# Performance work log

Hardware: AMD Instinct MI355X
Metric: run time of the kernel (lower is better)

Reference implementation:

```python
import jax, jax.numpy as jnp
import numpy as np

N, NF1, NF2, NH, OUT, K = 16384, 2000, 10000, 512, 16, 19
BN_EPS = 1e-5

def _bn(x, g, b, m, v):
    # eval-mode BatchNorm1d with running stats
    return (x - m) * jax.lax.rsqrt(v + BN_EPS) * g + b


def setup_inputs() -> dict:
    key = jax.random.key(0)
    ks = jax.random.split(key, 24)
    f32 = jnp.float32
    def w(k, shape):
        return jax.random.normal(k, shape, f32) * 0.02
    inp = {
        "rna": jax.random.normal(ks[0], (N, NF1), f32),
        "atac": jax.random.normal(ks[1], (N, NF2), f32),
        "index_rna": jnp.arange(N, dtype=jnp.int32),
        "index_atac": jnp.arange(N, dtype=jnp.int32),
        "eps": jax.random.normal(ks[2], (N, OUT), f32),
        # RNA encoder
        "W_r1": w(ks[3], (NH, NF1)), "b_r1": jnp.zeros((NH,), f32),
        "g_r": jnp.ones((NH,), f32), "be_r": jnp.zeros((NH,), f32),
        "m_r": jnp.zeros((NH,), f32), "v_r": jnp.ones((NH,), f32),
        "W_rmu": w(ks[4], (OUT, NH)), "b_rmu": jnp.zeros((OUT,), f32),
        "W_rvar": w(ks[5], (OUT, NH)), "b_rvar": jnp.zeros((OUT,), f32),
        # ATAC encoder
        "W_a1": w(ks[6], (NH, NF2)), "b_a1": jnp.zeros((NH,), f32),
        "g_a": jnp.ones((NH,), f32), "be_a": jnp.zeros((NH,), f32),
        "m_a": jnp.zeros((NH,), f32), "v_a": jnp.ones((NH,), f32),
        "W_amu": w(ks[7], (OUT, NH)), "b_amu": jnp.zeros((OUT,), f32),
        "W_avar": w(ks[8], (OUT, NH)), "b_avar": jnp.zeros((OUT,), f32),
        # decoder
        "W_d1": w(ks[9], (NH, OUT)), "b_d1": jnp.zeros((NH,), f32),
        "g_d": jnp.ones((NH,), f32), "be_d": jnp.zeros((NH,), f32),
        "m_d": jnp.zeros((NH,), f32), "v_d": jnp.ones((NH,), f32),
        "W_d4": w(ks[10], (NF1 + NF2, NH)), "b_d4": jnp.zeros((NF1 + NF2,), f32),
        "cluster": jax.random.normal(ks[11], (K, OUT), f32),
    }
    return inp


def reference(rna, atac, index_rna, index_atac, eps,
              W_r1, b_r1, g_r, be_r, m_r, v_r, W_rmu, b_rmu, W_rvar, b_rvar,
              W_a1, b_a1, g_a, be_a, m_a, v_a, W_amu, b_amu, W_avar, b_avar,
              W_d1, b_d1, g_d, be_d, m_d, v_d, W_d4, b_d4, cluster):
    n = rna.shape[0]
    # encoders (dropout is identity in eval mode)
    h_rna = jax.nn.relu(_bn(rna @ W_r1.T + b_r1, g_r, be_r, m_r, v_r))
    zm_rna = h_rna @ W_rmu.T + b_rmu
    zv_rna = jnp.exp(h_rna @ W_rvar.T + b_rvar)
    h_atac = jax.nn.relu(_bn(atac @ W_a1.T + b_a1, g_a, be_a, m_a, v_a))
    zm_atac = h_atac @ W_amu.T + b_amu
    zv_atac = jnp.exp(h_atac @ W_avar.T + b_avar)
    # vectorized scatter replacing the per-sample Python loop
    mu = jnp.ones((n, 2, OUT), rna.dtype)
    var = jnp.ones((n, 2, OUT), rna.dtype)
    mask = jnp.zeros((n, 2, OUT), rna.dtype)
    mu = mu.at[index_rna, 0].set(zm_rna).at[index_atac, 1].set(zm_atac)
    var = var.at[index_rna, 0].set(zv_rna).at[index_atac, 1].set(zv_atac)
    mask = mask.at[index_rna, 0].set(1.0).at[index_atac, 1].set(1.0)
    # product of experts over the modality axis (axis=1)
    T = mask / var
    T_sum = T.sum(axis=1) + 1.0            # [n, OUT]
    z_mu = (mu * T).sum(axis=1) / T_sum
    z_var = 1.0 / T_sum
    # Normal(z_mu, scale=z_var).rsample() with externally supplied eps
    z = z_mu + z_var * eps
    # student-t style soft assignment to clusters
    d2 = jnp.sum((z[:, None, :] - cluster[None, :, :]) ** 2, axis=2)  # [n, K]
    q = 1.0 / (1.0 + d2)
    q = q / q.sum(axis=1, keepdims=True)
    # decoder
    h = jax.nn.relu(_bn(z @ W_d1.T + b_d1, g_d, be_d, m_d, v_d))
    recon_x = h @ W_d4.T + b_d4
    return (recon_x, z_mu, z_var, z, q)
```

## Files before the change

kernel.cpp:

```cpp
#include <hip/hip_runtime.h>

#define NS   16384
#define NF1c 2000
#define NF2c 10000
#define NH   512
#define KC   19
#define NREC 12000

typedef short bf16x8 __attribute__((ext_vector_type(8)));
typedef float f32x4  __attribute__((ext_vector_type(4)));

__device__ __forceinline__ unsigned short f2bf(float x) {
    unsigned int u = __builtin_bit_cast(unsigned int, x);
    u += 0x7FFFu + ((u >> 16) & 1u);
    return (unsigned short)(u >> 16);
}
__device__ __forceinline__ float bf2f(unsigned short h) {
    return __builtin_bit_cast(float, (unsigned int)h << 16);
}

__global__ void k_cvt(const float* __restrict__ s, unsigned short* __restrict__ d, int n4) {
    int i = blockIdx.x * blockDim.x + threadIdx.x;
    int st = gridDim.x * blockDim.x;
    for (; i < n4; i += st) {
        float4 f = ((const float4*)s)[i];
        ushort4 o;
        o.x = f2bf(f.x); o.y = f2bf(f.y); o.z = f2bf(f.z); o.w = f2bf(f.w);
        ((ushort4*)d)[i] = o;
    }
}

__global__ void k_prep_st(const float* __restrict__ g, const float* __restrict__ be,
                          const float* __restrict__ m, const float* __restrict__ v,
                          const float* __restrict__ b1,
                          float* __restrict__ s, float* __restrict__ t, int n) {
    int i = blockIdx.x * blockDim.x + threadIdx.x;
    if (i < n) {
        float sc = g[i] * rsqrtf(v[i] + 1e-5f);
        s[i] = sc;
        t[i] = be[i] + (b1[i] - m[i]) * sc;
    }
}

__global__ void k_zero(float* __restrict__ p, int n) {
    int i = blockIdx.x * blockDim.x + threadIdx.x;
    if (i < n) p[i] = 0.f;
}

template<int EPI, int A_BF16>
__global__ __launch_bounds__(256)
void k_gemm(const void* __restrict__ Aptr, const unsigned short* __restrict__ B,
            int K, int Nn,
            const float* __restrict__ sc, const float* __restrict__ sh,
            unsigned short* __restrict__ Hout, float* __restrict__ Fout)
{
    __shared__ __align__(16) unsigned short As[128 * 32];
    __shared__ __align__(16) unsigned short Bs[128 * 32];
    const int tid  = threadIdx.x;
    const int tn   = blockIdx.x, tm = blockIdx.y;
    const int wave = tid >> 6, lane = tid & 63;
    const int wr   = wave >> 1, wc = wave & 1;
    const int lo   = lane & 15, hi = lane >> 4;
    const int srow = tid >> 1, shalf = tid & 1;
    const long arow = (long)tm * 128 + srow;
    const int  brow = tn * 128 + srow;

    f32x4 acc[4][4];
#pragma unroll
    for (int i = 0; i < 4; i++)
#pragma unroll
        for (int j = 0; j < 4; j++) acc[i][j] = (f32x4){0.f, 0.f, 0.f, 0.f};

    char* Ab = (char*)As;
    char* Bb = (char*)Bs;
    const int wc0 = (srow << 6) + ((((shalf * 2)    ) ^ ((srow >> 1) & 3)) << 4);
    const int wc1 = (srow << 6) + ((((shalf * 2) + 1) ^ ((srow >> 1) & 3)) << 4);

    for (int k0 = 0; k0 < K; k0 += 32) {
        __syncthreads();
        const int kb = k0 + shalf * 16;
        {
            __align__(16) unsigned short u[16];
            if (A_BF16) {
                const unsigned short* ap = (const unsigned short*)Aptr + arow * (long)K + kb;
                *(uint4*)&u[0] = *(const uint4*)(ap);
                *(uint4*)&u[8] = *(const uint4*)(ap + 8);
            } else {
                const float* ap = (const float*)Aptr + arow * (long)K + kb;
                if (kb + 16 <= K) {
#pragma unroll
                    for (int q = 0; q < 4; q++) {
                        float4 f = ((const float4*)ap)[q];
                        u[q*4+0] = f2bf(f.x); u[q*4+1] = f2bf(f.y);
                        u[q*4+2] = f2bf(f.z); u[q*4+3] = f2bf(f.w);
                    }
                } else {
#pragma unroll
                    for (int j = 0; j < 16; j++)
                        u[j] = (kb + j < K) ? f2bf(ap[j]) : (unsigned short)0;
                }
            }
            *(uint4*)(Ab + wc0) = *(uint4*)&u[0];
            *(uint4*)(Ab + wc1) = *(uint4*)&u[8];
        }
        {
            uint4 q0 = {0, 0, 0, 0}, q1 = {0, 0, 0, 0};
            if (brow < Nn && kb < K) {
                const unsigned short* bp = B + (long)brow * K + kb;
                if (kb + 16 <= K) {
                    q0 = *(const uint4*)bp;
                    q1 = *(const uint4*)(bp + 8);
                } else {
                    __align__(16) unsigned short tb[16];
#pragma unroll
                    for (int j = 0; j < 16; j++)
                        tb[j] = (kb + j < K) ? bp[j] : (unsigned short)0;
                    q0 = *(uint4*)&tb[0]; q1 = *(uint4*)&tb[8];
                }
            }
            *(uint4*)(Bb + wc0) = q0;
            *(uint4*)(Bb + wc1) = q1;
        }
        __syncthreads();
        bf16x8 af[4], bfr[4];
#pragma unroll
        for (int f = 0; f < 4; f++) {
            int ar = wr * 64 + f * 16 + lo;
            af[f]  = *(const bf16x8*)(Ab + (ar << 6) + ((hi ^ ((ar >> 1) & 3)) << 4));
            int br = wc * 64 + f * 16 + lo;
            bfr[f] = *(const bf16x8*)(Bb + (br << 6) + ((hi ^ ((br >> 1) & 3)) << 4));
        }
#pragma unroll
        for (int i = 0; i < 4; i++)
#pragma unroll
            for (int j = 0; j < 4; j++)
                acc[i][j] = __builtin_amdgcn_mfma_f32_16x16x32_bf16(af[i], bfr[j], acc[i][j], 0, 0, 0);
    }
#pragma unroll
    for (int i = 0; i < 4; i++) {
#pragma unroll
        for (int j = 0; j < 4; j++) {
            const int col = tn * 128 + wc * 64 + j * 16 + lo;
#pragma unroll
            for (int r = 0; r < 4; r++) {
                const long row = (long)tm * 128 + wr * 64 + i * 16 + hi * 4 + r;
                float v = acc[i][j][r];
                if (EPI == 0) {
                    v = fmaxf(v * sc[col] + sh[col], 0.f);
                    Hout[row * NH + col] = f2bf(v);
                } else {
                    if (col < Nn) Fout[row * (long)Nn + col] = v + sc[col];
                }
            }
        }
    }
}

__global__ __launch_bounds__(256)
void k_proj(const unsigned short* __restrict__ h_rna,
            const unsigned short* __restrict__ h_atac,
            const float* __restrict__ W_rmu, const float* __restrict__ b_rmu,
            const float* __restrict__ W_rvar, const float* __restrict__ b_rvar,
            const float* __restrict__ W_amu, const float* __restrict__ b_amu,
            const float* __restrict__ W_avar, const float* __restrict__ b_avar,
            const int* __restrict__ idx_rna, const int* __restrict__ idx_atac,
            float* __restrict__ mu0, float* __restrict__ var0,
            float* __restrict__ mu1, float* __restrict__ var1,
            float* __restrict__ mflag)
{
    __shared__ __align__(16) unsigned short hsh[4][2][NH];
    const int wave = threadIdx.x >> 6, lane = threadIdx.x & 63;
    const long i = (long)blockIdx.x * 4 + wave;
    *(uint4*)&hsh[wave][0][lane * 8] = *(const uint4*)(h_rna  + i * NH + lane * 8);
    *(uint4*)&hsh[wave][1][lane * 8] = *(const uint4*)(h_atac + i * NH + lane * 8);
    __syncthreads();
    const int mod = lane >> 5, oo = lane & 31;
    const int isv = oo >> 4, o = oo & 15;
    const float *W, *bias;
    if (mod == 0) { W = isv ? W_rvar : W_rmu; bias = isv ? b_rvar : b_rmu; }
    else          { W = isv ? W_avar : W_amu; bias = isv ? b_avar : b_amu; }
    const unsigned short* hr = hsh[wave][mod];
    const float* wrow = W + o * NH;
    float a = 0.f;
#pragma unroll 4
    for (int k = 0; k < NH; k += 4) {
        float4 w = *(const float4*)(wrow + k);
        a += bf2f(hr[k]) * w.x + bf2f(hr[k+1]) * w.y + bf2f(hr[k+2]) * w.z + bf2f(hr[k+3]) * w.w;
    }
    a += bias[o];
    const int tgt = (mod == 0) ? idx_rna[i] : idx_atac[i];
    float* mu  = mod ? mu1  : mu0;
    float* var = mod ? var1 : var0;
    if (!isv) mu[(long)tgt * 16 + o] = a;
    else      var[(long)tgt * 16 + o] = expf(a);
    if (oo == 0) mflag[(long)mod * NS + tgt] = 1.f;
}

__global__ __launch_bounds__(256)
void k_combine(const float* __restrict__ mu0, const float* __restrict__ var0,
               const float* __restrict__ mu1, const float* __restrict__ var1,
               const float* __restrict__ mflag,
               const float* __restrict__ eps, const float* __restrict__ cluster,
               const float* __restrict__ W_d1,
               const float* __restrict__ s_d, const float* __restrict__ t_d,
               float* __restrict__ o_zmu, float* __restrict__ o_zvar,
               float* __restrict__ o_z, float* __restrict__ o_q,
               unsigned short* __restrict__ h_d)
{
    __shared__ float zsh[4][16];
    const int wave = threadIdx.x >> 6, lane = threadIdx.x & 63;
    const long i = (long)blockIdx.x * 4 + wave;
    if (lane < 16) {
        const int d = lane;
        const float f0 = mflag[i], f1 = mflag[NS + i];
        float ts = 1.f, num = 0.f;
        if (f0 != 0.f) { float iv = 1.f / var0[i*16+d]; ts += iv; num += mu0[i*16+d] * iv; }
        if (f1 != 0.f) { float iv = 1.f / var1[i*16+d]; ts += iv; num += mu1[i*16+d] * iv; }
        const float zm = num / ts, zv = 1.f / ts;
        const float z = zm + zv * eps[i*16+d];
        o_zmu[i*16+d] = zm; o_zvar[i*16+d] = zv; o_z[i*16+d] = z;
        zsh[wave][d] = z;
    }
    __syncthreads();
    float zreg[16];
#pragma unroll
    for (int d = 0; d < 16; d++) zreg[d] = zsh[wave][d];
    float qk = 0.f;
    if (lane < KC) {
        float d2 = 0.f;
#pragma unroll
        for (int d = 0; d < 16; d++) { float df = zreg[d] - cluster[lane*16+d]; d2 += df*df; }
        qk = 1.f / (1.f + d2);
    }
    float ssum = qk;
#pragma unroll
    for (int off = 16; off > 0; off >>= 1) ssum += __shfl_xor(ssum, off, 32);
    if (lane < KC) o_q[i * KC + lane] = qk / ssum;
#pragma unroll
    for (int j = 0; j < 8; j++) {
        const int c = lane + 64 * j;
        float a = 0.f;
#pragma unroll
        for (int d = 0; d < 16; d += 4) {
            float4 w = *(const float4*)(W_d1 + c * 16 + d);
            a += zreg[d] * w.x + zreg[d+1] * w.y + zreg[d+2] * w.z + zreg[d+3] * w.w;
        }
        a = fmaxf(a * s_d[c] + t_d[c], 0.f);
        h_d[i * NH + c] = f2bf(a);
    }
}

extern "C" void kernel_launch(void* const* d_in, const int* in_sizes, int n_in,
                              void* d_out, int out_size, void* d_ws, size_t ws_size,
                              hipStream_t stream)
{
    const float* rna    = (const float*)d_in[0];
    const float* atac   = (const float*)d_in[1];
    const int*   i_rna  = (const int*)d_in[2];
    const int*   i_atac = (const int*)d_in[3];
    const float* eps    = (const float*)d_in[4];
    const float* W_r1   = (const float*)d_in[5];
    const float* b_r1   = (const float*)d_in[6];
    const float* g_r    = (const float*)d_in[7];
    const float* be_r   = (const float*)d_in[8];
    const float* m_r    = (const float*)d_in[9];
    const float* v_r    = (const float*)d_in[10];
    const float* W_rmu  = (const float*)d_in[11];
    const float* b_rmu  = (const float*)d_in[12];
    const float* W_rvar = (const float*)d_in[13];
    const float* b_rvar = (const float*)d_in[14];
    const float* W_a1   = (const float*)d_in[15];
    const float* b_a1   = (const float*)d_in[16];
    const float* g_a    = (const float*)d_in[17];
    const float* be_a   = (const float*)d_in[18];
    const float* m_a    = (const float*)d_in[19];
    const float* v_a    = (const float*)d_in[20];
    const float* W_amu  = (const float*)d_in[21];
    const float* b_amu  = (const float*)d_in[22];
    const float* W_avar = (const float*)d_in[23];
    const float* b_avar = (const float*)d_in[24];
    const float* W_d1   = (const float*)d_in[25];
    const float* b_d1   = (const float*)d_in[26];
    const float* g_d    = (const float*)d_in[27];
    const float* be_d   = (const float*)d_in[28];
    const float* m_d    = (const float*)d_in[29];
    const float* v_d    = (const float*)d_in[30];
    const float* W_d4   = (const float*)d_in[31];
    const float* b_d4   = (const float*)d_in[32];
    const float* clus   = (const float*)d_in[33];
    (void)in_sizes; (void)n_in; (void)out_size;

    char* w = (char*)d_ws;
    size_t off = 0;
    auto carve = [&](size_t bytes) { void* p = w + off; off += (bytes + 255) & ~(size_t)255; return p; };
    unsigned short* wr1b  = (unsigned short*)carve((size_t)NH * NF1c * 2);
    unsigned short* wa1b  = (unsigned short*)carve((size_t)NH * NF2c * 2);
    unsigned short* wd4b  = (unsigned short*)carve((size_t)NREC * NH * 2);
    unsigned short* hrna  = (unsigned short*)carve((size_t)NS * NH * 2);
    unsigned short* hatac = (unsigned short*)carve((size_t)NS * NH * 2);
    unsigned short* hd    = (unsigned short*)carve((size_t)NS * NH * 2);
    float* mu0   = (float*)carve((size_t)NS * 16 * 4);
    float* var0  = (float*)carve((size_t)NS * 16 * 4);
    float* mu1   = (float*)carve((size_t)NS * 16 * 4);
    float* var1  = (float*)carve((size_t)NS * 16 * 4);
    float* mflag = (float*)carve((size_t)2 * NS * 4);
    float* st    = (float*)carve((size_t)6 * NH * 4);
    if (off > ws_size) return;

    float* s_r = st;          float* t_r = st + NH;
    float* s_a = st + 2*NH;   float* t_a = st + 3*NH;
    float* s_d = st + 4*NH;   float* t_d = st + 5*NH;

    float* out    = (float*)d_out;
    float* o_rec  = out;
    float* o_zmu  = out + (size_t)NS * NREC;
    float* o_zvar = o_zmu + (size_t)NS * 16;
    float* o_z    = o_zvar + (size_t)NS * 16;
    float* o_q    = o_z + (size_t)NS * 16;

    k_cvt<<<1024, 256, 0, stream>>>(W_r1, wr1b, NH * NF1c / 4);
    k_cvt<<<2048, 256, 0, stream>>>(W_a1, wa1b, NH * NF2c / 4);
    k_cvt<<<2048, 256, 0, stream>>>(W_d4, wd4b, NREC * NH / 4);
    k_prep_st<<<2, 256, 0, stream>>>(g_r, be_r, m_r, v_r, b_r1, s_r, t_r, NH);
    k_prep_st<<<2, 256, 0, stream>>>(g_a, be_a, m_a, v_a, b_a1, s_a, t_a, NH);
    k_prep_st<<<2, 256, 0, stream>>>(g_d, be_d, m_d, v_d, b_d1, s_d, t_d, NH);
    k_zero<<<(2 * NS + 255) / 256, 256, 0, stream>>>(mflag, 2 * NS);

    dim3 blk(256);
    dim3 ge(4, 128);
    k_gemm<0, 0><<<ge, blk, 0, stream>>>(rna,  wr1b, NF1c, NH, s_r, t_r, hrna,  nullptr);
    k_gemm<0, 0><<<ge, blk, 0, stream>>>(atac, wa1b, NF2c, NH, s_a, t_a, hatac, nullptr);
    k_proj<<<NS / 4, blk, 0, stream>>>(hrna, hatac, W_rmu, b_rmu, W_rvar, b_rvar,
                                       W_amu, b_amu, W_avar, b_avar, i_rna, i_atac,
                                       mu0, var0, mu1, var1, mflag);
    k_combine<<<NS / 4, blk, 0, stream>>>(mu0, var0, mu1, var1, mflag, eps, clus,
                                          W_d1, s_d, t_d, o_zmu, o_zvar, o_z, o_q, hd);
    dim3 gd(94, 128);
    k_gemm<1, 1><<<gd, blk, 0, stream>>>(hd, wd4b, NH, NREC, b_d4, nullptr, nullptr, o_rec);
}
```

Baseline: 1.437 ms.

## Double-buffer GEMM LDS tiles with register prefetch and XCD-aware block remap

The GEMM kernel now keeps two LDS buffers and prefetches the next K-tile from global memory into registers while the current tile is being computed, dropping one barrier per iteration. The launch becomes a 1D grid, and block indices are remapped so consecutive logical tiles land on the same XCD (stride of eight) for better L2 reuse of the A and B panels. The cost is more LDS and registers per block, which may reduce occupancy. The remap assumes the grid size is divisible by eight; 512 and 94*128 both are.

```diff
diff --git a/kernel.cpp b/kernel.cpp
--- a/kernel.cpp
+++ b/kernel.cpp
@@ -50,14 +50,18 @@
 template<int EPI, int A_BF16>
 __global__ __launch_bounds__(256)
 void k_gemm(const void* __restrict__ Aptr, const unsigned short* __restrict__ B,
-            int K, int Nn,
+            int K, int Nn, int ntn,
             const float* __restrict__ sc, const float* __restrict__ sh,
             unsigned short* __restrict__ Hout, float* __restrict__ Fout)
 {
-    __shared__ __align__(16) unsigned short As[128 * 32];
-    __shared__ __align__(16) unsigned short Bs[128 * 32];
+    __shared__ __align__(16) unsigned short As[2][128 * 32];
+    __shared__ __align__(16) unsigned short Bs[2][128 * 32];
+    const int nwg = gridDim.x;
+    const int q8  = nwg >> 3;
+    const int L   = (blockIdx.x & 7) * q8 + (blockIdx.x >> 3);
+    const int tn  = L % ntn, tm = L / ntn;
+
     const int tid  = threadIdx.x;
-    const int tn   = blockIdx.x, tm = blockIdx.y;
     const int wave = tid >> 6, lane = tid & 63;
     const int wr   = wave >> 1, wc = wave & 1;
     const int lo   = lane & 15, hi = lane >> 4;
@@ -71,57 +75,67 @@
 #pragma unroll
         for (int j = 0; j < 4; j++) acc[i][j] = (f32x4){0.f, 0.f, 0.f, 0.f};
 
-    char* Ab = (char*)As;
-    char* Bb = (char*)Bs;
     const int wc0 = (srow << 6) + ((((shalf * 2)    ) ^ ((srow >> 1) & 3)) << 4);
     const int wc1 = (srow << 6) + ((((shalf * 2) + 1) ^ ((srow >> 1) & 3)) << 4);
 
-    for (int k0 = 0; k0 < K; k0 += 32) {
-        __syncthreads();
+    float4 rfa[4];
+    uint4  ra0, ra1;
+    uint4  rb0, rb1;
+
+    auto issue_load = [&](int k0) {
         const int kb = k0 + shalf * 16;
-        {
-            __align__(16) unsigned short u[16];
-            if (A_BF16) {
-                const unsigned short* ap = (const unsigned short*)Aptr + arow * (long)K + kb;
-                *(uint4*)&u[0] = *(const uint4*)(ap);
-                *(uint4*)&u[8] = *(const uint4*)(ap + 8);
+        if (A_BF16) {
+            const unsigned short* ap = (const unsigned short*)Aptr + arow * (long)K + kb;
+            ra0 = *(const uint4*)ap;
+            ra1 = *(const uint4*)(ap + 8);
+        } else {
+            const float* ap = (const float*)Aptr + arow * (long)K + kb;
+            if (kb + 16 <= K) {
+                rfa[0] = ((const float4*)ap)[0];
+                rfa[1] = ((const float4*)ap)[1];
+                rfa[2] = ((const float4*)ap)[2];
+                rfa[3] = ((const float4*)ap)[3];
             } else {
-                const float* ap = (const float*)Aptr + arow * (long)K + kb;
-                if (kb + 16 <= K) {
-#pragma unroll
-                    for (int q = 0; q < 4; q++) {
-                        float4 f = ((const float4*)ap)[q];
-                        u[q*4+0] = f2bf(f.x); u[q*4+1] = f2bf(f.y);
-                        u[q*4+2] = f2bf(f.z); u[q*4+3] = f2bf(f.w);
-                    }
-                } else {
-#pragma unroll
-                    for (int j = 0; j < 16; j++)
-                        u[j] = (kb + j < K) ? f2bf(ap[j]) : (unsigned short)0;
-                }
+#pragma unroll
+                for (int j = 0; j < 16; j++)
+                    ((float*)rfa)[j] = (kb + j < K) ? ap[j] : 0.f;
             }
-            *(uint4*)(Ab + wc0) = *(uint4*)&u[0];
-            *(uint4*)(Ab + wc1) = *(uint4*)&u[8];
-        }
-        {
-            uint4 q0 = {0, 0, 0, 0}, q1 = {0, 0, 0, 0};
-            if (brow < Nn && kb < K) {
-                const unsigned short* bp = B + (long)brow * K + kb;
-                if (kb + 16 <= K) {
-                    q0 = *(const uint4*)bp;
-                    q1 = *(const uint4*)(bp + 8);
-                } else {
-                    __align__(16) unsigned short tb[16];
-#pragma unroll
-                    for (int j = 0; j < 16; j++)
-                        tb[j] = (kb + j < K) ? bp[j] : (unsigned short)0;
-                    q0 = *(uint4*)&tb[0]; q1 = *(uint4*)&tb[8];
-                }
+        }
+        rb0 = (uint4){0, 0, 0, 0}; rb1 = (uint4){0, 0, 0, 0};
+        if (brow < Nn && kb < K) {
+            const unsigned short* bp = B + (long)brow * K + kb;
+            if (kb + 16 <= K) {
+                rb0 = *(const uint4*)bp;
+                rb1 = *(const uint4*)(bp + 8);
+            } else {
+                __align__(16) unsigned short tb[16];
+#pragma unroll
+                for (int j = 0; j < 16; j++)
+                    tb[j] = (kb + j < K) ? bp[j] : (unsigned short)0;
+                rb0 = *(uint4*)&tb[0]; rb1 = *(uint4*)&tb[8];
             }
-            *(uint4*)(Bb + wc0) = q0;
-            *(uint4*)(Bb + wc1) = q1;
-        }
-        __syncthreads();
+        }
+    };
+
+    auto write_lds = [&](int buf) {
+        char* Ab = (char*)As[buf];
+        char* Bb = (char*)Bs[buf];
+        __align__(16) unsigned short u[16];
+        if (A_BF16) {
+            *(uint4*)&u[0] = ra0; *(uint4*)&u[8] = ra1;
+        } else {
+#pragma unroll
+            for (int j = 0; j < 16; j++) u[j] = f2bf(((const float*)rfa)[j]);
+        }
+        *(uint4*)(Ab + wc0) = *(uint4*)&u[0];
+        *(uint4*)(Ab + wc1) = *(uint4*)&u[8];
+        *(uint4*)(Bb + wc0) = rb0;
+        *(uint4*)(Bb + wc1) = rb1;
+    };
+
+    auto compute = [&](int buf) {
+        char* Ab = (char*)As[buf];
+        char* Bb = (char*)Bs[buf];
         bf16x8 af[4], bfr[4];
 #pragma unroll
         for (int f = 0; f < 4; f++) {
@@ -135,7 +149,17 @@
 #pragma unroll
             for (int j = 0; j < 4; j++)
                 acc[i][j] = __builtin_amdgcn_mfma_f32_16x16x32_bf16(af[i], bfr[j], acc[i][j], 0, 0, 0);
-    }
+    };
+
+    const int nt = (K + 31) / 32;
+    issue_load(0);
+    for (int t = 0; t < nt; ++t) {
+        write_lds(t & 1);
+        if (t + 1 < nt) issue_load((t + 1) * 32);
+        __syncthreads();
+        compute(t & 1);
+    }
+
 #pragma unroll
     for (int i = 0; i < 4; i++) {
 #pragma unroll
@@ -327,14 +351,12 @@
     k_zero<<<(2 * NS + 255) / 256, 256, 0, stream>>>(mflag, 2 * NS);
 
     dim3 blk(256);
-    dim3 ge(4, 128);
-    k_gemm<0, 0><<<ge, blk, 0, stream>>>(rna,  wr1b, NF1c, NH, s_r, t_r, hrna,  nullptr);
-    k_gemm<0, 0><<<ge, blk, 0, stream>>>(atac, wa1b, NF2c, NH, s_a, t_a, hatac, nullptr);
+    k_gemm<0, 0><<<512, blk, 0, stream>>>(rna,  wr1b, NF1c, NH, 4, s_r, t_r, hrna,  nullptr);
+    k_gemm<0, 0><<<512, blk, 0, stream>>>(atac, wa1b, NF2c, NH, 4, s_a, t_a, hatac, nullptr);
     k_proj<<<NS / 4, blk, 0, stream>>>(hrna, hatac, W_rmu, b_rmu, W_rvar, b_rvar,
                                        W_amu, b_amu, W_avar, b_avar, i_rna, i_atac,
                                        mu0, var0, mu1, var1, mflag);
     k_combine<<<NS / 4, blk, 0, stream>>>(mu0, var0, mu1, var1, mflag, eps, clus,
                                           W_d1, s_d, t_d, o_zmu, o_zvar, o_z, o_q, hd);
-    dim3 gd(94, 128);
-    k_gemm<1, 1><<<gd, blk, 0, stream>>>(hd, wd4b, NH, NREC, b_d4, nullptr, nullptr, o_rec);
-}
+    k_gemm<1, 1><<<94 * 128, blk, 0, stream>>>(hd, wd4b, NH, NREC, 94, b_d4, nullptr, nullptr, o_rec);
+}
```

Measured after the change: 1.461 ms. About the same (+1.7%).
